# Performance work log

Hardware: AMD Instinct MI355X
Metric: run time of the kernel (lower is better)

The kernel has to match this reference:

```python
import jax, jax.numpy as jnp
import numpy as np

LN_EPS = 1e-5
BN_EPS = 1e-5


def lstm_scan(x, Wih, Whh, b, reverse=False):
    # x: [T, B, D]; Wih: [4H, D]; Whh: [4H, H]; b: [4H]
    H = Whh.shape[1]
    xg = jnp.einsum('tbd,gd->tbg', x, Wih) + b  # [T, B, 4H]
    if reverse:
        xg = xg[::-1]

    def step(carry, g_x):
        h, c = carry
        g = g_x + h @ Whh.T
        i, f, gg, o = jnp.split(g, 4, axis=-1)
        c = jax.nn.sigmoid(f) * c + jax.nn.sigmoid(i) * jnp.tanh(gg)
        h = jax.nn.sigmoid(o) * jnp.tanh(c)
        return (h, c), h

    B = x.shape[1]
    h0 = jnp.zeros((B, H), x.dtype)
    _, hs = jax.lax.scan(step, (h0, h0), xg)
    if reverse:
        hs = hs[::-1]
    return hs  # [T, B, H]


def layernorm(x, g, b):
    mu = jnp.mean(x, axis=-1, keepdims=True)
    var = jnp.mean(jnp.square(x - mu), axis=-1, keepdims=True)
    return (x - mu) * jax.lax.rsqrt(var + LN_EPS) * g + b


def setup_inputs() -> dict:
    key = jax.random.key(0)
    ks = jax.random.split(key, 16)
    B, T, E, H = 256, 256, 128, 128
    H2 = 2 * H
    s = 0.1  # weight init scale
    return {
        'inp_embed': jax.random.normal(ks[0], (B, T, E), jnp.float32),
        'inp_last_idx': jax.random.randint(ks[1], (B,), 0, T, jnp.int64),
        'Wih_f': s * jax.random.normal(ks[2], (4 * H, E), jnp.float32),
        'Whh_f': s * jax.random.normal(ks[3], (4 * H, H), jnp.float32),
        'b_f': s * jax.random.normal(ks[4], (4 * H,), jnp.float32),
        'Wih_r': s * jax.random.normal(ks[5], (4 * H, E), jnp.float32),
        'Whh_r': s * jax.random.normal(ks[6], (4 * H, H), jnp.float32),
        'b_r': s * jax.random.normal(ks[7], (4 * H,), jnp.float32),
        'ln1_g': jnp.ones((H2,), jnp.float32),
        'ln1_b': jnp.zeros((H2,), jnp.float32),
        'W1ih': s * jax.random.normal(ks[8], (4 * H2, H2), jnp.float32),
        'W1hh': s * jax.random.normal(ks[9], (4 * H2, H2), jnp.float32),
        'b1': s * jax.random.normal(ks[10], (4 * H2,), jnp.float32),
        'ln2_g': jnp.ones((H2,), jnp.float32),
        'ln2_b': jnp.zeros((H2,), jnp.float32),
        'W2ih': s * jax.random.normal(ks[11], (4 * H2, H2), jnp.float32),
        'W2hh': s * jax.random.normal(ks[12], (4 * H2, H2), jnp.float32),
        'b2': s * jax.random.normal(ks[13], (4 * H2,), jnp.float32),
        'bn_g': jnp.ones((H2,), jnp.float32),
        'bn_b': jnp.zeros((H2,), jnp.float32),
    }


def reference(inp_embed, inp_last_idx, Wih_f, Whh_f, b_f, Wih_r, Whh_r, b_r,
              ln1_g, ln1_b, W1ih, W1hh, b1, ln2_g, ln2_b, W2ih, W2hh, b2,
              bn_g, bn_b):
    # eval mode: dropouts are identity, batchnorm uses running stats (mean=0, var=1)
    x = jnp.transpose(inp_embed, (1, 0, 2))  # [T, B, E]
    h_fwd = lstm_scan(x, Wih_f, Whh_f, b_f, reverse=False)
    h_bwd = lstm_scan(x, Wih_r, Whh_r, b_r, reverse=True)
    bilstm_out = jnp.concatenate([h_fwd, h_bwd], axis=-1)  # [T, B, 2H]
    bilstm_out = layernorm(bilstm_out, ln1_g, ln1_b)
    lstm_out = lstm_scan(bilstm_out, W1ih, W1hh, b1)
    lstm_out = layernorm(lstm_out + bilstm_out, ln2_g, ln2_b)
    lstm_out = lstm_scan(lstm_out, W2ih, W2hh, b2)  # [T, B, 2H]
    # gather last valid timestep per batch element
    gathered = lstm_out[inp_last_idx, jnp.arange(lstm_out.shape[1])]  # [B, 2H]
    y = (gathered * jax.lax.rsqrt(jnp.float32(1.0 + BN_EPS))) * bn_g + bn_b
    return jax.nn.relu(y)
```

## Files before the change

kernel.cpp:

```cpp
#include <hip/hip_runtime.h>
#include <cstdint>
#include <cstddef>

typedef unsigned short u16;
typedef unsigned long long u64;
typedef __attribute__((ext_vector_type(8))) short bf16x8;
typedef __attribute__((ext_vector_type(4))) float f32x4;
typedef __attribute__((ext_vector_type(4))) unsigned short u16x4;

#define DEV __device__ __forceinline__

DEV float bf2f(u16 h) { union { unsigned int u; float f; } x; x.u = ((unsigned int)h) << 16; return x.f; }
DEV u16 f2bf(float f) {
    union { float f; unsigned int u; } x; x.f = f;
    unsigned int u = x.u;
    return (u16)((u + 0x7fffu + ((u >> 16) & 1u)) >> 16);
}
DEV float fsig(float x)  { float e = __expf(-x);      return __builtin_amdgcn_rcpf(1.0f + e); }
DEV float ftanh(float x) { float e = __expf(2.0f * x); return 1.0f - 2.0f * __builtin_amdgcn_rcpf(e + 1.0f); }
DEV f32x4 mfma16(bf16x8 a, bf16x8 b, f32x4 c) {
    return __builtin_amdgcn_mfma_f32_16x16x32_bf16(a, b, c, 0, 0, 0);
}


union __align__(16) SMemU {
    struct { u16 As[64][40]; u16 Bs[128][40]; } g;
    struct { u16 Al[2][16][136]; } r1;
    struct { u16 Al[16][264]; } r2;
};

__global__ __launch_bounds__(256) void prep_w4_kernel(
    const float* __restrict__ a0, u16* __restrict__ o0, int c0,
    const float* __restrict__ a1, u16* __restrict__ o1, int c1,
    const float* __restrict__ a2, u16* __restrict__ o2, int c2,
    const float* __restrict__ a3, u16* __restrict__ o3)
{
    int blk = blockIdx.x;
    const float* a; u16* o; int off;
    if (blk < c0)                { a = a0; o = o0; off = blk; }
    else if (blk < c0 + c1)      { a = a1; o = o1; off = blk - c0; }
    else if (blk < c0 + c1 + c2) { a = a2; o = o2; off = blk - c0 - c1; }
    else                         { a = a3; o = o3; off = blk - c0 - c1 - c2; }
    int i = off * 256 + threadIdx.x;
    o[i] = f2bf(a[i]);
}

__global__ __launch_bounds__(256) void prep_x1_kernel(
    float* __restrict__ X, const float* __restrict__ gw, const float* __restrict__ bw)
{
    int row  = blockIdx.x * 4 + (threadIdx.x >> 6);
    int lane = threadIdx.x & 63;
    float* xr = X + (size_t)row * 256;
    f32x4 v = *(const f32x4*)(xr + lane * 4);
    float s = v[0] + v[1] + v[2] + v[3];
    #pragma unroll
    for (int mm = 1; mm < 64; mm <<= 1) s += __shfl_xor(s, mm, 64);
    float mu = s * (1.0f / 256.0f);
    f32x4 e = v - mu;
    float q = e[0]*e[0] + e[1]*e[1] + e[2]*e[2] + e[3]*e[3];
    #pragma unroll
    for (int mm = 1; mm < 64; mm <<= 1) q += __shfl_xor(q, mm, 64);
    float rs = rsqrtf(q * (1.0f / 256.0f) + 1e-5f);
    int c0 = lane * 4;
    u16x4 hv, lv;
    #pragma unroll
    for (int i = 0; i < 4; ++i) {
        float o = e[i] * rs * gw[c0 + i] + bw[c0 + i];
        u16 hh = f2bf(o);
        hv[i] = hh;
        lv[i] = f2bf(o - bf2f(hh));
    }
    u16* H = (u16*)xr;
    *(u16x4*)(H + lane * 4)       = hv;
    *(u16x4*)(H + 256 + lane * 4) = lv;
}

DEV void xg_fr_body(SMemU* smu, int bx, int by, int nby,
    const float* __restrict__ embed,
    const u16* __restrict__ Wf16, const float* __restrict__ bf_,
    const u16* __restrict__ Wr16, const float* __restrict__ br_,
    float* __restrict__ xgf, float* __restrict__ xgr, int t0f, int t0r)
{
    auto& As = smu->g.As;
    auto& Bs = smu->g.Bs;
    int tid = threadIdx.x;
    int half = nby >> 1;
    bool isR = by >= half;
    int m0 = (by - (isR ? half : 0)) * 64;
    const u16* W      = isR ? Wr16 : Wf16;
    const float* bias = isR ? br_ : bf_;
    float* out        = isR ? xgr : xgf;
    int tbase         = isR ? t0r : t0f;
    int n0 = bx * 64;

    int r  = tid >> 2;
    int kc = (tid & 3) * 8;
    int m  = m0 + r;
    int tl = m >> 8, bb = m & 255;
    const float* arow = embed + ((size_t)(bb * 256 + (tbase + tl)) * 128);
    const u16* brow = W + ((size_t)(n0 + r) * 128);

    f32x4 acc[4];
    #pragma unroll
    for (int i = 0; i < 4; ++i) acc[i] = (f32x4){0.f, 0.f, 0.f, 0.f};
    int lane = tid & 63, w = tid >> 6;
    int fr_ = lane & 15, kb0 = (lane >> 4) * 8;

    for (int kt = 0; kt < 8; ++kt) {
        int sc = (kt & 3) * 32 + kc;
        bool lo = kt >= 4;
        f32x4 va = *(const f32x4*)(arow + sc);
        f32x4 vb = *(const f32x4*)(arow + sc + 4);
        bf16x8 wv = *(const bf16x8*)(brow + sc);
        bf16x8 hv;
        #pragma unroll
        for (int i = 0; i < 8; ++i) {
            float v = (i < 4) ? va[i] : vb[i - 4];
            u16 hi = f2bf(v);
            hv[i] = (short)(lo ? f2bf(v - bf2f(hi)) : hi);
        }
        *(bf16x8*)&As[r][kc] = hv;
        *(bf16x8*)&Bs[r][kc] = wv;
        __syncthreads();
        bf16x8 bfrg = *(const bf16x8*)&Bs[w * 16 + fr_][kb0];
        #pragma unroll
        for (int mt = 0; mt < 4; ++mt) {
            bf16x8 afrg = *(const bf16x8*)&As[mt * 16 + fr_][kb0];
            acc[mt] = mfma16(afrg, bfrg, acc[mt]);
        }
        __syncthreads();
    }
    int col = n0 + w * 16 + fr_;
    float bvv = bias[col];
    int rq = (lane >> 4) * 4;
    #pragma unroll
    for (int mt = 0; mt < 4; ++mt)
        #pragma unroll
        for (int rr = 0; rr < 4; ++rr) {
            int mrow = m0 + mt * 16 + rq + rr;
            out[(size_t)mrow * 512 + col] = acc[mt][rr] + bvv;
        }
}

DEV void xg_l16_body(SMemU* smu, int bx, int by,
    const u16* __restrict__ X1p, const u16* __restrict__ Wp,
    const float* __restrict__ bias, float* __restrict__ out, int t0)
{
    auto& As = smu->g.As;
    auto& Bs = smu->g.Bs;
    int tid = threadIdx.x;
    int m0 = by * 64, n0 = bx * 128;
    int rA = tid >> 2, kcA = (tid & 3) * 8;
    int rB = tid >> 1, kcB = (tid & 1) * 16;
    int m  = m0 + rA;
    int tl = m >> 8, bb = m & 255;
    const u16* arow = X1p + ((size_t)((t0 + tl) * 256 + bb)) * 512;
    const u16* brow = Wp + ((size_t)(n0 + rB)) * 256;

    f32x4 acc[2][4];
    #pragma unroll
    for (int cs = 0; cs < 2; ++cs)
        #pragma unroll
        for (int i = 0; i < 4; ++i) acc[cs][i] = (f32x4){0.f, 0.f, 0.f, 0.f};
    int lane = tid & 63, w = tid >> 6;
    int fr_ = lane & 15, kb0 = (lane >> 4) * 8;

    for (int kt = 0; kt < 16; ++kt) {
        int sc = (kt & 7) * 32;
        bf16x8 hv  = *(const bf16x8*)(arow + ((kt >= 8) ? 256 : 0) + sc + kcA);
        bf16x8 wv0 = *(const bf16x8*)(brow + sc + kcB);
        bf16x8 wv1 = *(const bf16x8*)(brow + sc + kcB + 8);
        *(bf16x8*)&As[rA][kcA] = hv;
        *(bf16x8*)&Bs[rB][kcB] = wv0;
        *(bf16x8*)&Bs[rB][kcB + 8] = wv1;
        __syncthreads();
        bf16x8 b0 = *(const bf16x8*)&Bs[w * 16 + fr_][kb0];
        bf16x8 b1 = *(const bf16x8*)&Bs[64 + w * 16 + fr_][kb0];
        #pragma unroll
        for (int mt = 0; mt < 4; ++mt) {
            bf16x8 afrg = *(const bf16x8*)&As[mt * 16 + fr_][kb0];
            acc[0][mt] = mfma16(afrg, b0, acc[0][mt]);
            acc[1][mt] = mfma16(afrg, b1, acc[1][mt]);
        }
        __syncthreads();
    }
    int rq = (lane >> 4) * 4;
    #pragma unroll
    for (int cs = 0; cs < 2; ++cs) {
        int col = n0 + cs * 64 + w * 16 + fr_;
        float bvv = bias[col];
        #pragma unroll
        for (int mt = 0; mt < 4; ++mt)
            #pragma unroll
            for (int rr = 0; rr < 4; ++rr) {
                int mrow = m0 + mt * 16 + rq + rr;
                out[(size_t)mrow * 1024 + col] = acc[cs][mt][rr] + bvv;
            }
    }
}

DEV void xg_ln3_body(SMemU* smu, int bx, int by,
    const u16* __restrict__ X1p, const float* __restrict__ Rc,
    const float* __restrict__ l2g, const float* __restrict__ l2b,
    const u16* __restrict__ Wp, const float* __restrict__ bias,
    float* __restrict__ out, int t0)
{
    auto& As = smu->g.As;
    auto& Bs = smu->g.Bs;
    int tid = threadIdx.x;
    int m0 = by * 64, n0 = bx * 128;
    int rA = tid >> 2, kcA = (tid & 3) * 8;
    int rB = tid >> 1, kcB = (tid & 1) * 16;
    int m  = m0 + rA;
    int tl = m >> 8, bb = m & 255;
    const u16* a1 = X1p + ((size_t)((t0 + tl) * 256 + bb)) * 512;
    const float* a2 = Rc + ((size_t)(tl * 256 + bb)) * 256;
    const u16* brow = Wp + ((size_t)(n0 + rB)) * 256;

    float xc[8][8];
    float s = 0.f;
    #pragma unroll
    for (int q = 0; q < 8; ++q) {
        int sc = q * 32 + kcA;
        bf16x8 hx = *(const bf16x8*)(a1 + sc);
        bf16x8 lx = *(const bf16x8*)(a1 + 256 + sc);
        f32x4 u2 = *(const f32x4*)(a2 + sc);
        f32x4 v2 = *(const f32x4*)(a2 + sc + 4);
        #pragma unroll
        for (int i = 0; i < 8; ++i) {
            float rv = (i < 4) ? u2[i] : v2[i - 4];
            xc[q][i] = bf2f((u16)hx[i]) + bf2f((u16)lx[i]) + rv;
            s += xc[q][i];
        }
    }
    s += __shfl_xor(s, 1); s += __shfl_xor(s, 2);
    float mu = s * (1.0f / 256.0f);
    float q2 = 0.f;
    #pragma unroll
    for (int q = 0; q < 8; ++q)
        #pragma unroll
        for (int i = 0; i < 8; ++i) { float e = xc[q][i] - mu; q2 += e * e; }
    q2 += __shfl_xor(q2, 1); q2 += __shfl_xor(q2, 2);
    float rs = rsqrtf(q2 * (1.0f / 256.0f) + 1e-5f);
    #pragma unroll
    for (int q = 0; q < 8; ++q) {
        int sc = q * 32 + kcA;
        f32x4 g1 = *(const f32x4*)(l2g + sc);
        f32x4 g2v = *(const f32x4*)(l2g + sc + 4);
        f32x4 h1 = *(const f32x4*)(l2b + sc);
        f32x4 h2 = *(const f32x4*)(l2b + sc + 4);
        #pragma unroll
        for (int i = 0; i < 4; ++i) {
            xc[q][i]     = (xc[q][i]     - mu) * rs * g1[i]  + h1[i];
            xc[q][4 + i] = (xc[q][4 + i] - mu) * rs * g2v[i] + h2[i];
        }
    }

    f32x4 acc[2][4];
    #pragma unroll
    for (int cs = 0; cs < 2; ++cs)
        #pragma unroll
        for (int i = 0; i < 4; ++i) acc[cs][i] = (f32x4){0.f, 0.f, 0.f, 0.f};
    int lane = tid & 63, w = tid >> 6;
    int fr_ = lane & 15, kb0 = (lane >> 4) * 8;

    #pragma unroll
    for (int kt = 0; kt < 16; ++kt) {
        int q = kt & 7, sc = q * 32;
        bool lo = kt >= 8;
        bf16x8 wv0 = *(const bf16x8*)(brow + sc + kcB);
        bf16x8 wv1 = *(const bf16x8*)(brow + sc + kcB + 8);
        bf16x8 hv;
        #pragma unroll
        for (int i = 0; i < 8; ++i) {
            float v = xc[q][i];
            u16 hi = f2bf(v);
            hv[i] = (short)(lo ? f2bf(v - bf2f(hi)) : hi);
        }
        *(bf16x8*)&As[rA][kcA] = hv;
        *(bf16x8*)&Bs[rB][kcB] = wv0;
        *(bf16x8*)&Bs[rB][kcB + 8] = wv1;
        __syncthreads();
        bf16x8 b0 = *(const bf16x8*)&Bs[w * 16 + fr_][kb0];
        bf16x8 b1 = *(const bf16x8*)&Bs[64 + w * 16 + fr_][kb0];
        #pragma unroll
        for (int mt = 0; mt < 4; ++mt) {
            bf16x8 afrg = *(const bf16x8*)&As[mt * 16 + fr_][kb0];
            acc[0][mt] = mfma16(afrg, b0, acc[0][mt]);
            acc[1][mt] = mfma16(afrg, b1, acc[1][mt]);
        }
        __syncthreads();
    }
    int rq = (lane >> 4) * 4;
    #pragma unroll
    for (int cs = 0; cs < 2; ++cs) {
        int col = n0 + cs * 64 + w * 16 + fr_;
        float bvv = bias[col];
        #pragma unroll
        for (int mt = 0; mt < 4; ++mt)
            #pragma unroll
            for (int rr = 0; rr < 4; ++rr) {
                int mrow = m0 + mt * 16 + rq + rr;
                out[(size_t)mrow * 1024 + col] = acc[cs][mt][rr] + bvv;
            }
    }
}

DEV void recur1_body(SMemU* smu, int bid,
    const float* __restrict__ xgf, const float* __restrict__ xgr,
    const u16* __restrict__ whf16, const u16* __restrict__ whr16,
    float* __restrict__ cbf, float* __restrict__ cbr,
    float* __restrict__ hpf, float* __restrict__ hpr,
    float* __restrict__ xout, int s0, int s1)
{
    __builtin_amdgcn_s_setprio(1);
    constexpr int K = 128, N4 = 512;
    auto& Al = smu->r1.Al;

    int tid = threadIdx.x, lane = tid & 63, w = tid >> 6;
    int fr_ = lane & 15, quad = lane >> 4, kb0 = quad * 8;
    int dir = bid >> 5, gidx = bid & 31;
    const float* xg  = dir ? xgr  : xgf;
    const u16* whh16 = dir ? whr16 : whf16;
    float* cb = dir ? cbr : cbf;
    float* hp = dir ? hpr : hpf;
    int coloff = dir ? 128 : 0;

    bf16x8 bf[4][2][4];
    #pragma unroll
    for (int g = 0; g < 4; ++g)
        #pragma unroll
        for (int u = 0; u < 2; ++u) {
            const u16* src = whh16 + (size_t)(g * K + w * 32 + u * 16 + fr_) * K;
            #pragma unroll
            for (int kt = 0; kt < 4; ++kt)
                bf[g][u][kt] = *(const bf16x8*)(src + kt * 32 + kb0);
        }

    int uq = quad >> 1, qrow = quad & 1;
    int colw = w * 32 + uq * 16 + fr_;
    int b0 = gidx * 8;
    float c[4];
    #pragma unroll
    for (int rr = 0; rr < 4; ++rr)
        c[rr] = (s0 > 0) ? cb[(size_t)(b0 + qrow * 4 + rr) * K + colw] : 0.f;

    if (s0 > 0) {
        for (int idx = tid; idx < 8 * K; idx += 256) {
            int sa = idx >> 7, k = idx & 127;
            float v = hp[(size_t)(b0 + sa) * K + k];
            u16 hh = f2bf(v);
            Al[s0 & 1][sa][k] = hh;
            Al[s0 & 1][8 + sa][k] = f2bf(v - bf2f(hh));
        }
    }
    __syncthreads();

    float xv[4][4];
    {
        int xrow = dir ? (s1 - 1 - s0) : 0;
        #pragma unroll
        for (int rr = 0; rr < 4; ++rr) {
            const float* xp = xg + ((size_t)(xrow * 256 + b0 + qrow * 4 + rr)) * N4 + colw;
            #pragma unroll
            for (int g = 0; g < 4; ++g) xv[rr][g] = xp[g * K];
        }
    }

    for (int t = s0; t < s1; ++t) {
        float xn[4][4];
        {
            int tn = (t + 1 < s1) ? (t + 1) : t;
            int xrow = dir ? (s1 - 1 - tn) : (tn - s0);
            #pragma unroll
            for (int rr = 0; rr < 4; ++rr) {
                const float* xp = xg + ((size_t)(xrow * 256 + b0 + qrow * 4 + rr)) * N4 + colw;
                #pragma unroll
                for (int g = 0; g < 4; ++g) xn[rr][g] = xp[g * K];
            }
        }
        f32x4 acc[4][2];
        if (t > 0) {
            #pragma unroll
            for (int g = 0; g < 4; ++g)
                #pragma unroll
                for (int u = 0; u < 2; ++u) acc[g][u] = (f32x4){0.f, 0.f, 0.f, 0.f};
            #pragma unroll
            for (int kt = 0; kt < 4; ++kt) {
                bf16x8 a = *(const bf16x8*)&Al[t & 1][fr_][kt * 32 + kb0];
                #pragma unroll
                for (int g = 0; g < 4; ++g)
                    #pragma unroll
                    for (int u = 0; u < 2; ++u) acc[g][u] = mfma16(a, bf[g][u][kt], acc[g][u]);
            }
            #pragma unroll
            for (int g = 0; g < 4; ++g)
                #pragma unroll
                for (int u = 0; u < 2; ++u)
                    #pragma unroll
                    for (int rr = 0; rr < 4; ++rr)
                        acc[g][u][rr] += __shfl_xor(acc[g][u][rr], 32);
        }
        int tt = dir ? (255 - t) : t;
        #pragma unroll
        for (int rr = 0; rr < 4; ++rr) {
            int s = qrow * 4 + rr;
            float gg[4];
            #pragma unroll
            for (int g = 0; g < 4; ++g) {
                float pv = (t > 0) ? (uq ? acc[g][1][rr] : acc[g][0][rr]) : 0.f;
                gg[g] = xv[rr][g] + pv;
            }
            c[rr] = fsig(gg[1]) * c[rr] + fsig(gg[0]) * ftanh(gg[2]);
            float h = fsig(gg[3]) * ftanh(c[rr]);
            u16 hh = f2bf(h);
            Al[(t + 1) & 1][s][colw] = hh;
            Al[(t + 1) & 1][8 + s][colw] = f2bf(h - bf2f(hh));
            xout[((size_t)tt * 256 + b0 + s) * 256 + coloff + colw] = h;
            if (t == s1 - 1) hp[(size_t)(b0 + s) * K + colw] = h;
        }
        __syncthreads();
        #pragma unroll
        for (int rr = 0; rr < 4; ++rr)
            #pragma unroll
            for (int g = 0; g < 4; ++g) xv[rr][g] = xn[rr][g];
    }
    #pragma unroll
    for (int rr = 0; rr < 4; ++rr)
        cb[(size_t)(b0 + qrow * 4 + rr) * K + colw] = c[rr];
}

template<int OUTY>
DEV void recur2_body(SMemU* smu, int bid,
    const float* __restrict__ xg, const u16* __restrict__ whh16,
    float* __restrict__ cb, u64* hb,
    float* __restrict__ xoutc, float* __restrict__ yout,
    const int* __restrict__ lastidx,
    const float* __restrict__ bng, const float* __restrict__ bnb,
    int s0, int s1)
{
    __builtin_amdgcn_s_setprio(1);
    constexpr int K = 256, MB = 8, N4 = 1024;
    constexpr int CNT = MB * K / 256;
    auto& Al = smu->r2.Al;

    int tid = threadIdx.x, lane = tid & 63, w = tid >> 6;
    int fr_ = lane & 15, quad = lane >> 4, kb0 = quad * 8;
    int group = bid >> 2, cw = bid & 3;
    u64* hbg = hb + (size_t)group * (2 * MB * K);
    int col = cw * 64 + w * 16 + fr_;

    bf16x8 bf[4][8];
    #pragma unroll
    for (int g = 0; g < 4; ++g) {
        const u16* src = whh16 + (size_t)(g * 256 + col) * K;
        #pragma unroll
        for (int kt = 0; kt < 8; ++kt)
            bf[g][kt] = *(const bf16x8*)(src + kt * 32 + kb0);
    }

    int qrow = quad & 1, rhalf = quad >> 1;
    int sp[2], bs[2]; float c[2];
    #pragma unroll
    for (int j = 0; j < 2; ++j) {
        sp[j] = qrow * 4 + rhalf * 2 + j;
        bs[j] = group * 8 + sp[j];
        c[j] = (s0 > 0) ? cb[(size_t)bs[j] * K + col] : 0.f;
    }
    int lastb[2] = { -1, -1 };
    float bngv = 0.f, bnbv = 0.f;
    if (OUTY) {
        bool is64 = (lastidx[1] | lastidx[3] | lastidx[5] | lastidx[7] |
                     lastidx[9] | lastidx[11] | lastidx[13] | lastidx[15]) == 0;
        lastb[0] = is64 ? lastidx[2 * bs[0]] : lastidx[bs[0]];
        lastb[1] = is64 ? lastidx[2 * bs[1]] : lastidx[bs[1]];
        bngv = bng[col] * rsqrtf(1.0f + 1e-5f);
        bnbv = bnb[col];
    }

    float xv[2][4];
    #pragma unroll
    for (int j = 0; j < 2; ++j) {
        const float* xp = xg + ((size_t)bs[j]) * N4 + col;
        #pragma unroll
        for (int g = 0; g < 4; ++g) xv[j][g] = xp[g * 256];
    }

    for (int t = s0; t < s1; ++t) {
        float xn[2][4];
        {
            int tn = (t + 1 < s1) ? (t + 1) : t;
            int xr = tn - s0;
            #pragma unroll
            for (int j = 0; j < 2; ++j) {
                const float* xp = xg + ((size_t)(xr * 256 + bs[j])) * N4 + col;
                #pragma unroll
                for (int g = 0; g < 4; ++g) xn[j][g] = xp[g * 256];
            }
        }
        f32x4 acc[4];
        if (t > 0) {
            u64* hsrc = hbg + (size_t)(t & 1) * (MB * K);
            u64 v[CNT];
            #pragma unroll
            for (int i = 0; i < CNT; ++i)
                v[i] = __hip_atomic_load(hsrc + tid + i * 256,
                                         __ATOMIC_RELAXED, __HIP_MEMORY_SCOPE_AGENT);
            for (;;) {
                bool ok = true;
                #pragma unroll
                for (int i = 0; i < CNT; ++i)
                    if ((unsigned int)(v[i] >> 32) != (unsigned int)t) ok = false;
                if (ok) break;
                __builtin_amdgcn_s_sleep(1);
                #pragma unroll
                for (int i = 0; i < CNT; ++i)
                    if ((unsigned int)(v[i] >> 32) != (unsigned int)t)
                        v[i] = __hip_atomic_load(hsrc + tid + i * 256,
                                                 __ATOMIC_RELAXED, __HIP_MEMORY_SCOPE_AGENT);
            }
            #pragma unroll
            for (int i = 0; i < CNT; ++i) {
                unsigned int d = (unsigned int)v[i];
                Al[i][tid]     = (u16)(d & 0xffffu);
                Al[8 + i][tid] = (u16)(d >> 16);
            }
            __syncthreads();
            #pragma unroll
            for (int g = 0; g < 4; ++g) acc[g] = (f32x4){0.f, 0.f, 0.f, 0.f};
            #pragma unroll
            for (int kt = 0; kt < 8; ++kt) {
                bf16x8 a = *(const bf16x8*)&Al[fr_][kt * 32 + kb0];
                #pragma unroll
                for (int g = 0; g < 4; ++g) acc[g] = mfma16(a, bf[g][kt], acc[g]);
            }
            #pragma unroll
            for (int g = 0; g < 4; ++g)
                #pragma unroll
                for (int rr = 0; rr < 4; ++rr)
                    acc[g][rr] += __shfl_xor(acc[g][rr], 32);
        }
        #pragma unroll
        for (int j = 0; j < 2; ++j) {
            float gg[4];
            #pragma unroll
            for (int g = 0; g < 4; ++g) {
                float pv = (t > 0) ? (rhalf ? acc[g][2 + j] : acc[g][j]) : 0.f;
                gg[g] = xv[j][g] + pv;
            }
            c[j] = fsig(gg[1]) * c[j] + fsig(gg[0]) * ftanh(gg[2]);
            float h = fsig(gg[3]) * ftanh(c[j]);
            u16 hh = f2bf(h);
            u16 hl = f2bf(h - bf2f(hh));
            u64 word = (u64)((unsigned int)hh | ((unsigned int)hl << 16))
                     | ((u64)(unsigned int)(t + 1) << 32);
            __hip_atomic_store(hbg + (size_t)((t + 1) & 1) * (MB * K) + (size_t)sp[j] * K + col,
                               word, __ATOMIC_RELAXED, __HIP_MEMORY_SCOPE_AGENT);
            if (OUTY == 0) {
                xoutc[((size_t)(t - s0) * 256 + bs[j]) * 256 + col] = h;
            } else if (t == lastb[j]) {
                float y = h * bngv + bnbv;
                y = y > 0.f ? y : 0.f;
                yout[(size_t)bs[j] * 256 + col] = y;
            }
        }
        #pragma unroll
        for (int j = 0; j < 2; ++j)
            #pragma unroll
            for (int g = 0; g < 4; ++g) xv[j][g] = xn[j][g];
    }
    #pragma unroll
    for (int j = 0; j < 2; ++j) cb[(size_t)bs[j] * K + col] = c[j];
}

__global__ __launch_bounds__(256) void fused1_kernel(
    const float* __restrict__ embed,
    const u16* __restrict__ Wf16, const float* __restrict__ bfb,
    const u16* __restrict__ Wr16, const float* __restrict__ brb,
    float* __restrict__ xgfw, float* __restrict__ xgrw, int t0f, int t0r, int gon,
    const float* __restrict__ xgfr, const float* __restrict__ xgrr,
    const u16* __restrict__ whf16, const u16* __restrict__ whr16,
    float* __restrict__ cbf, float* __restrict__ cbr,
    float* __restrict__ hpf, float* __restrict__ hpr,
    float* __restrict__ X1, int s0, int s1, int ron)
{
    __shared__ SMemU sm;
    int b = blockIdx.x;
    if (b < 64) {
        if (ron)
            recur1_body(&sm, b, xgfr, xgrr, whf16, whr16, cbf, cbr, hpf, hpr, X1, s0, s1);
    } else {
        if (gon) {
            int idx = b - 64;
            xg_fr_body(&sm, idx & 7, idx >> 3, 256, embed, Wf16, bfb, Wr16, brb,
                       xgfw, xgrw, t0f, t0r);
        }
    }
}

__global__ __launch_bounds__(256) void fused2_kernel(
    const float* __restrict__ xg2, const u16* __restrict__ wh1,
    float* __restrict__ cb1, u64* hb1, float* __restrict__ Rw,
    int s2a, int s2b, int s2on,
    const float* __restrict__ xg3, const u16* __restrict__ wh2,
    float* __restrict__ cb2, u64* hb2, float* __restrict__ yout,
    const int* __restrict__ lastidx, const float* __restrict__ bng,
    const float* __restrict__ bnb, int s3a, int s3b, int s3on,
    const u16* __restrict__ X1p, const u16* __restrict__ w1p,
    const float* __restrict__ b1, float* __restrict__ G2w, int g2t0, int g2on,
    const float* __restrict__ Rr, const float* __restrict__ ln2g,
    const float* __restrict__ ln2b, const u16* __restrict__ w2p,
    const float* __restrict__ b2v, float* __restrict__ G3w, int g3t0, int g3on)
{
    __shared__ SMemU sm;
    int b = blockIdx.x;
    if (b < 256) {
        int x = b & 7, k = b >> 3;
        int sub = k & 15;
        int gid = (x * 4 + (sub >> 2)) * 4 + (sub & 3);
        if (k < 16) {
            if (s2on)
                recur2_body<0>(&sm, gid, xg2, wh1, cb1, hb1, Rw,
                               nullptr, nullptr, nullptr, nullptr, s2a, s2b);
        } else {
            if (s3on)
                recur2_body<1>(&sm, gid, xg3, wh2, cb2, hb2,
                               nullptr, yout, lastidx, bng, bnb, s3a, s3b);
        }
    } else if (b < 768) {
        if (g2on) {
            int i = b - 256;
            xg_l16_body(&sm, i & 7, i >> 3, X1p, w1p, b1, G2w, g2t0);
        }
    } else {
        if (g3on) {
            int i = b - 768;
            xg_ln3_body(&sm, i & 7, i >> 3, X1p, Rr, ln2g, ln2b, w2p, b2v, G3w, g3t0);
        }
    }
}

__global__ __launch_bounds__(256) void xg2_kernel(
    const u16* __restrict__ X1p, const u16* __restrict__ Wp,
    const float* __restrict__ bias, float* __restrict__ out, int t0)
{
    __shared__ SMemU sm;
    xg_l16_body(&sm, blockIdx.x, blockIdx.y, X1p, Wp, bias, out, t0);
}

extern "C" void kernel_launch(void* const* d_in, const int* in_sizes, int n_in,
                              void* d_out, int out_size, void* d_ws, size_t ws_size,
                              hipStream_t stream)
{
    (void)in_sizes; (void)n_in; (void)out_size; (void)ws_size;
    const float* embed = (const float*)d_in[0];
    const int* lastidx = (const int*)d_in[1];
    const float* Wih_f = (const float*)d_in[2];
    const float* Whh_f = (const float*)d_in[3];
    const float* b_f   = (const float*)d_in[4];
    const float* Wih_r = (const float*)d_in[5];
    const float* Whh_r = (const float*)d_in[6];
    const float* b_r   = (const float*)d_in[7];
    const float* ln1g  = (const float*)d_in[8];
    const float* ln1b  = (const float*)d_in[9];
    const float* W1ih  = (const float*)d_in[10];
    const float* W1hh  = (const float*)d_in[11];
    const float* b1    = (const float*)d_in[12];
    const float* ln2g  = (const float*)d_in[13];
    const float* ln2b  = (const float*)d_in[14];
    const float* W2ih  = (const float*)d_in[15];
    const float* W2hh  = (const float*)d_in[16];
    const float* b2    = (const float*)d_in[17];
    const float* bng   = (const float*)d_in[18];
    const float* bnb   = (const float*)d_in[19];

    const size_t MiB = 1024 * 1024;
    char* ws = (char*)d_ws;
    float* G2[2] = { (float*)ws,               (float*)(ws + 16 * MiB) };
    float* G3[2] = { (float*)(ws + 32 * MiB),  (float*)(ws + 48 * MiB) };
    float* X1    =   (float*)(ws + 64 * MiB);
    float* R[2]  = { (float*)(ws + 128 * MiB), (float*)(ws + 132 * MiB) };
    char* p = ws + 136 * MiB;
    u64* hb1 = (u64*)p;                         p += 1024 * 1024;
    u64* hb2 = (u64*)p;                         p += 1024 * 1024;
    float* cbf = (float*)p;                     p += 128 * 1024;
    float* cbr = (float*)p;                     p += 128 * 1024;
    float* cb1 = (float*)p;                     p += 256 * 1024;
    float* cb2 = (float*)p;                     p += 256 * 1024;
    float* hpf = (float*)p;                     p += 128 * 1024;
    float* hpr = (float*)p;                     p += 128 * 1024;
    u16* w1p   = (u16*)p;                       p += 512 * 1024;
    u16* w2p   = (u16*)p;                       p += 512 * 1024;
    u16* wfp   = (u16*)p;                       p += 128 * 1024;
    u16* wrp   = (u16*)p;                       p += 128 * 1024;
    u16* wh1p  = (u16*)p;                       p += 512 * 1024;
    u16* wh2p  = (u16*)p;                       p += 512 * 1024;
    u16* whfp  = (u16*)p;                       p += 128 * 1024;
    u16* whrp  = (u16*)p;

    const int CH1 = 32, n1 = 8;
    const int CH  = 16, n2 = 16;

    prep_w4_kernel<<<2560, 256, 0, stream>>>(
        W1ih, w1p, 1024, W2ih, w2p, 1024, Wih_f, wfp, 256, Wih_r, wrp);
    prep_w4_kernel<<<2560, 256, 0, stream>>>(
        W1hh, wh1p, 1024, W2hh, wh2p, 1024, Whh_f, whfp, 256, Whh_r, whrp);

    for (int i = 0; i <= n1; ++i) {
        int gon = (i < n1), ron = (i >= 1);
        float* wf = (i & 1) ? G3[0] : G2[0];
        float* wr = (i & 1) ? G3[1] : G2[1];
        const float* rf = ((i - 1) & 1) ? G3[0] : G2[0];
        const float* rr_ = ((i - 1) & 1) ? G3[1] : G2[1];
        fused1_kernel<<<2112, 256, 0, stream>>>(
            embed, wfp, b_f, wrp, b_r, wf, wr, CH1 * i, 256 - CH1 * (i + 1), gon,
            rf, rr_, whfp, whrp, cbf, cbr, hpf, hpr, X1, CH1 * (i - 1), CH1 * i, ron);
    }

    prep_x1_kernel<<<16384, 256, 0, stream>>>(X1, ln1g, ln1b);
    const u16* X1p = (const u16*)X1;

    xg2_kernel<<<dim3(8, CH * 4), 256, 0, stream>>>(X1p, w1p, b1, G2[0], 0);
    for (int i = 0; i <= n2 + 1; ++i) {
        int s2on = (i < n2), s3on = (i >= 2);
        int g2on = (i + 1 < n2), g3on = (i >= 1 && i <= n2);
        fused2_kernel<<<1280, 256, 0, stream>>>(
            G2[i & 1], wh1p, cb1, hb1, R[i & 1], CH * i, CH * (i + 1), s2on,
            G3[(i - 2) & 1], wh2p, cb2, hb2, (float*)d_out, lastidx, bng, bnb,
            CH * (i - 2), CH * (i - 1), s3on,
            X1p, w1p, b1, G2[(i + 1) & 1], CH * (i + 1), g2on,
            R[(i - 1) & 1], ln2g, ln2b, w2p, b2, G3[(i - 1) & 1], CH * (i - 1), g3on);
    }
}
```

Measured before the change: 1.997 ms.

## Widen layer-2 input-gate GEMM tiles and process hi/lo splits together with swizzled LDS

The layer-2 input projection GEMM now computes a 64x256 output tile per block instead of 64x128. It handles the bf16 high and low halves of the activation in the same K step, so each weight fragment loaded from LDS is reused across both halves and more columns. The block count for that stage drops from 512 to 256 in the fused launch. The layer-3 LN+GEMM body also processes hi/lo together, and both bodies use an XOR-swizzled B layout in shared memory to reduce bank conflicts. Shared memory per block grows and per-thread accumulators double, which may lower occupancy, and fewer blocks may leave parts of the GPU idle.

```diff
diff --git a/kernel.cpp b/kernel.cpp
--- a/kernel.cpp
+++ b/kernel.cpp
@@ -24,7 +24,7 @@
 
 
 union __align__(16) SMemU {
-    struct { u16 As[64][40]; u16 Bs[128][40]; } g;
+    struct { u16 As[2][64][40]; u16 Bs[256][40]; } g;
     struct { u16 Al[2][16][136]; } r1;
     struct { u16 Al[16][264]; } r2;
 };
@@ -81,7 +81,7 @@
     const u16* __restrict__ Wr16, const float* __restrict__ br_,
     float* __restrict__ xgf, float* __restrict__ xgr, int t0f, int t0r)
 {
-    auto& As = smu->g.As;
+    auto& As = smu->g.As[0];
     auto& Bs = smu->g.Bs;
     int tid = threadIdx.x;
     int half = nby >> 1;
@@ -149,44 +149,58 @@
     auto& As = smu->g.As;
     auto& Bs = smu->g.Bs;
     int tid = threadIdx.x;
-    int m0 = by * 64, n0 = bx * 128;
+    int m0 = by * 64, n0 = bx * 256;
     int rA = tid >> 2, kcA = (tid & 3) * 8;
-    int rB = tid >> 1, kcB = (tid & 1) * 16;
     int m  = m0 + rA;
     int tl = m >> 8, bb = m & 255;
     const u16* arow = X1p + ((size_t)((t0 + tl) * 256 + bb)) * 512;
-    const u16* brow = Wp + ((size_t)(n0 + rB)) * 256;
-
-    f32x4 acc[2][4];
-    #pragma unroll
-    for (int cs = 0; cs < 2; ++cs)
+    const u16* brow = Wp + ((size_t)(n0 + tid)) * 256;
+    int swB = (tid >> 3) & 3;
+
+    f32x4 acc[4][4];
+    #pragma unroll
+    for (int cs = 0; cs < 4; ++cs)
         #pragma unroll
         for (int i = 0; i < 4; ++i) acc[cs][i] = (f32x4){0.f, 0.f, 0.f, 0.f};
     int lane = tid & 63, w = tid >> 6;
-    int fr_ = lane & 15, kb0 = (lane >> 4) * 8;
-
-    for (int kt = 0; kt < 16; ++kt) {
-        int sc = (kt & 7) * 32;
-        bf16x8 hv  = *(const bf16x8*)(arow + ((kt >= 8) ? 256 : 0) + sc + kcA);
-        bf16x8 wv0 = *(const bf16x8*)(brow + sc + kcB);
-        bf16x8 wv1 = *(const bf16x8*)(brow + sc + kcB + 8);
-        *(bf16x8*)&As[rA][kcA] = hv;
-        *(bf16x8*)&Bs[rB][kcB] = wv0;
-        *(bf16x8*)&Bs[rB][kcB + 8] = wv1;
+    int fr_ = lane & 15, quad = lane >> 4, kb0 = quad * 8;
+
+    for (int kt = 0; kt < 8; ++kt) {
+        int sc = kt * 32;
+        bf16x8 hvH = *(const bf16x8*)(arow + sc + kcA);
+        bf16x8 hvL = *(const bf16x8*)(arow + 256 + sc + kcA);
+        bf16x8 wv0 = *(const bf16x8*)(brow + sc);
+        bf16x8 wv1 = *(const bf16x8*)(brow + sc + 8);
+        bf16x8 wv2 = *(const bf16x8*)(brow + sc + 16);
+        bf16x8 wv3 = *(const bf16x8*)(brow + sc + 24);
+        *(bf16x8*)&As[0][rA][kcA] = hvH;
+        *(bf16x8*)&As[1][rA][kcA] = hvL;
+        *(bf16x8*)&Bs[tid][(0 ^ swB) * 8] = wv0;
+        *(bf16x8*)&Bs[tid][(1 ^ swB) * 8] = wv1;
+        *(bf16x8*)&Bs[tid][(2 ^ swB) * 8] = wv2;
+        *(bf16x8*)&Bs[tid][(3 ^ swB) * 8] = wv3;
         __syncthreads();
-        bf16x8 b0 = *(const bf16x8*)&Bs[w * 16 + fr_][kb0];
-        bf16x8 b1 = *(const bf16x8*)&Bs[64 + w * 16 + fr_][kb0];
-        #pragma unroll
-        for (int mt = 0; mt < 4; ++mt) {
-            bf16x8 afrg = *(const bf16x8*)&As[mt * 16 + fr_][kb0];
-            acc[0][mt] = mfma16(afrg, b0, acc[0][mt]);
-            acc[1][mt] = mfma16(afrg, b1, acc[1][mt]);
-        }
+        bf16x8 bfrg[4];
+        #pragma unroll
+        for (int cs = 0; cs < 4; ++cs) {
+            int Br = cs * 64 + w * 16 + fr_;
+            int g  = quad ^ ((Br >> 3) & 3);
+            bfrg[cs] = *(const bf16x8*)&Bs[Br][g * 8];
+        }
+        #pragma unroll
+        for (int h = 0; h < 2; ++h)
+            #pragma unroll
+            for (int mt = 0; mt < 4; ++mt) {
+                bf16x8 afrg = *(const bf16x8*)&As[h][mt * 16 + fr_][kb0];
+                #pragma unroll
+                for (int cs = 0; cs < 4; ++cs)
+                    acc[cs][mt] = mfma16(afrg, bfrg[cs], acc[cs][mt]);
+            }
         __syncthreads();
     }
     int rq = (lane >> 4) * 4;
     #pragma unroll
-    for (int cs = 0; cs < 2; ++cs) {
+    for (int cs = 0; cs < 4; ++cs) {
         int col = n0 + cs * 64 + w * 16 + fr_;
         float bvv = bias[col];
         #pragma unroll
@@ -210,12 +224,13 @@
     int tid = threadIdx.x;
     int m0 = by * 64, n0 = bx * 128;
     int rA = tid >> 2, kcA = (tid & 3) * 8;
-    int rB = tid >> 1, kcB = (tid & 1) * 16;
+    int rB = tid >> 1, cB = tid & 1;
     int m  = m0 + rA;
     int tl = m >> 8, bb = m & 255;
     const u16* a1 = X1p + ((size_t)((t0 + tl) * 256 + bb)) * 512;
     const float* a2 = Rc + ((size_t)(tl * 256 + bb)) * 256;
     const u16* brow = Wp + ((size_t)(n0 + rB)) * 256;
+    int swB = (rB >> 3) & 3;
 
     float xc[8][8];
     float s = 0.f;
@@ -262,33 +277,42 @@
         #pragma unroll
         for (int i = 0; i < 4; ++i) acc[cs][i] = (f32x4){0.f, 0.f, 0.f, 0.f};
     int lane = tid & 63, w = tid >> 6;
-    int fr_ = lane & 15, kb0 = (lane >> 4) * 8;
-
-    #pragma unroll
-    for (int kt = 0; kt < 16; ++kt) {
-        int q = kt & 7, sc = q * 32;
-        bool lo = kt >= 8;
-        bf16x8 wv0 = *(const bf16x8*)(brow + sc + kcB);
-        bf16x8 wv1 = *(const bf16x8*)(brow + sc + kcB + 8);
-        bf16x8 hv;
+    int fr_ = lane & 15, quad = lane >> 4, kb0 = quad * 8;
+
+    #pragma unroll
+    for (int kt = 0; kt < 8; ++kt) {
+        int sc = kt * 32;
+        bf16x8 wv0 = *(const bf16x8*)(brow + sc + cB * 16);
+        bf16x8 wv1 = *(const bf16x8*)(brow + sc + cB * 16 + 8);
+        bf16x8 hvH, hvL;
         #pragma unroll
         for (int i = 0; i < 8; ++i) {
-            float v = xc[q][i];
+            float v = xc[kt][i];
             u16 hi = f2bf(v);
-            hv[i] = (short)(lo ? f2bf(v - bf2f(hi)) : hi);
-        }
-        *(bf16x8*)&As[rA][kcA] = hv;
-        *(bf16x8*)&Bs[rB][kcB] = wv0;
-        *(bf16x8*)&Bs[rB][kcB + 8] = wv1;
+            hvH[i] = (short)hi;
+            hvL[i] = (short)f2bf(v - bf2f(hi));
+        }
+        *(bf16x8*)&As[0][rA][kcA] = hvH;
+        *(bf16x8*)&As[1][rA][kcA] = hvL;
+        *(bf16x8*)&Bs[rB][((2 * cB) ^ swB) * 8]     = wv0;
+        *(bf16x8*)&Bs[rB][((2 * cB + 1) ^ swB) * 8] = wv1;
         __syncthreads();
-        bf16x8 b0 = *(const bf16x8*)&Bs[w * 16 + fr_][kb0];
-        bf16x8 b1 = *(const bf16x8*)&Bs[64 + w * 16 + fr_][kb0];
-        #pragma unroll
-        for (int mt = 0; mt < 4; ++mt) {
-            bf16x8 afrg = *(const bf16x8*)&As[mt * 16 + fr_][kb0];
-            acc[0][mt] = mfma16(afrg, b0, acc[0][mt]);
-            acc[1][mt] = mfma16(afrg, b1, acc[1][mt]);
-        }
+        bf16x8 bfrg[2];
+        #pragma unroll
+        for (int cs = 0; cs < 2; ++cs) {
+            int Br = cs * 64 + w * 16 + fr_;
+            int g  = quad ^ ((Br >> 3) & 3);
+            bfrg[cs] = *(const bf16x8*)&Bs[Br][g * 8];
+        }
+        #pragma unroll
+        for (int h = 0; h < 2; ++h)
+            #pragma unroll
+            for (int mt = 0; mt < 4; ++mt) {
+                bf16x8 afrg = *(const bf16x8*)&As[h][mt * 16 + fr_][kb0];
+                #pragma unroll
+                for (int cs = 0; cs < 2; ++cs)
+                    acc[cs][mt] = mfma16(afrg, bfrg[cs], acc[cs][mt]);
+            }
         __syncthreads();
     }
     int rq = (lane >> 4) * 4;
@@ -627,14 +651,14 @@
                 recur2_body<1>(&sm, gid, xg3, wh2, cb2, hb2,
                                nullptr, yout, lastidx, bng, bnb, s3a, s3b);
         }
-    } else if (b < 768) {
+    } else if (b < 512) {
         if (g2on) {
             int i = b - 256;
-            xg_l16_body(&sm, i & 7, i >> 3, X1p, w1p, b1, G2w, g2t0);
+            xg_l16_body(&sm, i & 3, i >> 2, X1p, w1p, b1, G2w, g2t0);
         }
     } else {
         if (g3on) {
-            int i = b - 768;
+            int i = b - 512;
             xg_ln3_body(&sm, i & 7, i >> 3, X1p, Rr, ln2g, ln2b, w2p, b2v, G3w, g3t0);
         }
     }
@@ -720,11 +744,11 @@
     prep_x1_kernel<<<16384, 256, 0, stream>>>(X1, ln1g, ln1b);
     const u16* X1p = (const u16*)X1;
 
-    xg2_kernel<<<dim3(8, CH * 4), 256, 0, stream>>>(X1p, w1p, b1, G2[0], 0);
+    xg2_kernel<<<dim3(4, CH * 4), 256, 0, stream>>>(X1p, w1p, b1, G2[0], 0);
     for (int i = 0; i <= n2 + 1; ++i) {
         int s2on = (i < n2), s3on = (i >= 2);
         int g2on = (i + 1 < n2), g3on = (i >= 1 && i <= n2);
-        fused2_kernel<<<1280, 256, 0, stream>>>(
+        fused2_kernel<<<1024, 256, 0, stream>>>(
             G2[i & 1], wh1p, cb1, hb1, R[i & 1], CH * i, CH * (i + 1), s2on,
             G3[(i - 2) & 1], wh2p, cb2, hb2, (float*)d_out, lastidx, bng, bnb,
             CH * (i - 2), CH * (i - 1), s3on,
```

Measured after the change: 1.886 ms. 1.06x faster.
